# Performance work log

Hardware: AMD Instinct MI355X
Metric: run time of the kernel (lower is better)

The kernel has to match this reference:

```python
import jax, jax.numpy as jnp
import numpy as np

N, E = 20000, 320000
D, H, DFF, EDIM, L = 256, 8, 1024, 16, 4
C = D // H  # head dim = 32
INPUT_DIM, EMB_DIM = 64, 64
EPS = 1e-5


def ln(x, g, b):
    mu = jnp.mean(x, axis=-1, keepdims=True)
    var = jnp.mean((x - mu) ** 2, axis=-1, keepdims=True)
    return (x - mu) * jax.lax.rsqrt(var + EPS) * g + b


def segment_softmax(alpha, seg, num_segments):
    # alpha: [E, H], seg: [E] destination node ids
    m = jax.ops.segment_max(alpha, seg, num_segments=num_segments)
    m = jnp.where(jnp.isfinite(m), m, 0.0)
    ex = jnp.exp(alpha - m[seg])
    s = jax.ops.segment_sum(ex, seg, num_segments=num_segments)
    return ex / (s[seg] + 1e-16)


def transformer_conv(x, edge_attr, src, dst, Wq, bq, Wk, bk, Wv, bv, We, Wskip, bskip):
    # PyG TransformerConv: heads=H, concat=True, root_weight=True, beta=False
    q = (x @ Wq + bq).reshape(N, H, C)
    k = (x @ Wk + bk).reshape(N, H, C)
    v = (x @ Wv + bv).reshape(N, H, C)
    e = (edge_attr @ We).reshape(E, H, C)  # lin_edge has no bias
    kj = k[src] + e                         # [E,H,C]
    alpha = jnp.einsum('ehc,ehc->eh', q[dst], kj) / np.sqrt(C)
    alpha = segment_softmax(alpha, dst, N)  # softmax over incoming edges
    msg = (v[src] + e) * alpha[:, :, None]  # [E,H,C]
    out = jax.ops.segment_sum(msg, dst, num_segments=N).reshape(N, H * C)
    return out + x @ Wskip + bskip          # root/skip connection


def setup_inputs() -> dict:
    key = jax.random.key(0)
    ks = jax.random.split(key, 40)
    s = 0.02
    inp = {
        'input': jax.random.normal(ks[0], (N, INPUT_DIM), jnp.float32),
        'node_embedding': jax.random.normal(ks[1], (N, EMB_DIM), jnp.float32),
        'edge_attr': jax.random.normal(ks[2], (E, EDIM), jnp.float32),
        'edge_index': jax.random.randint(ks[3], (2, E), 0, N, jnp.int64)
          if jax.config.jax_enable_x64 else jax.random.randint(ks[3], (2, E), 0, N, jnp.int32),
        'Win': jax.random.normal(ks[4], (INPUT_DIM, D)) * s, 'b_in': jnp.zeros(D),
        'Wemb': jax.random.normal(ks[5], (EMB_DIM, D)) * s, 'bemb': jnp.zeros(D),
        'Wfus': jax.random.normal(ks[6], (3 * D, D)) * s, 'bfus': jnp.zeros(D),
        'Wq': jax.random.normal(ks[7], (L, D, D)) * s, 'bq': jnp.zeros((L, D)),
        'Wk': jax.random.normal(ks[8], (L, D, D)) * s, 'bk': jnp.zeros((L, D)),
        'Wv': jax.random.normal(ks[9], (L, D, D)) * s, 'bv': jnp.zeros((L, D)),
        'We': jax.random.normal(ks[10], (L, EDIM, D)) * s,
        'Wskip': jax.random.normal(ks[11], (L, D, D)) * s, 'bskip': jnp.zeros((L, D)),
        'n1g': jnp.ones((L, D)), 'n1b': jnp.zeros((L, D)),
        'W1f': jax.random.normal(ks[12], (L, D, DFF)) * s, 'b1f': jnp.zeros((L, DFF)),
        'W2f': jax.random.normal(ks[13], (L, DFF, D)) * s, 'b2f': jnp.zeros((L, D)),
        'n2g': jnp.ones((L, D)), 'n2b': jnp.zeros((L, D)),
        'fng': jnp.ones(D), 'fnb': jnp.zeros(D),
    }
    return inp


def reference(input, node_embedding, edge_attr, edge_index, Win, b_in, Wemb, bemb,
              Wfus, bfus, Wq, bq, Wk, bk, Wv, bv, We, Wskip, bskip, n1g, n1b,
              W1f, b1f, W2f, b2f, n2g, n2b, fng, fnb):
    src, dst = edge_index[0], edge_index[1]
    inp_proj = input @ Win + b_in           # [N,D]
    emb_proj = node_embedding @ Wemb + bemb  # [N,D]
    x = emb_proj
    for l in range(L):
        combined = jnp.concatenate([x, inp_proj, emb_proj], axis=-1)  # [N,3D]
        x = combined @ Wfus + bfus
        # layer: prenorm attn + residual, prenorm FFN + residual (dropout=0)
        xn = ln(x, n1g[l], n1b[l])
        x2 = transformer_conv(xn, edge_attr, src, dst, Wq[l], bq[l], Wk[l], bk[l],
                              Wv[l], bv[l], We[l], Wskip[l], bskip[l])
        x = x + x2
        xn = ln(x, n2g[l], n2b[l])
        x2 = jax.nn.relu(xn @ W1f[l] + b1f[l]) @ W2f[l] + b2f[l]
        x = x + x2
    return ln(x, fng, fnb)
```

## Files before the change

### kernel.cpp

```cpp
#include <hip/hip_runtime.h>
#include <math.h>

#define NN   20000
#define EE   320000
#define DD   256
#define HH   8
#define CC   32
#define DFFN 1024
#define LLAY 4
#define INDIM 64

typedef _Float16 f16;
typedef __attribute__((ext_vector_type(8))) _Float16 f16x8;
typedef __attribute__((ext_vector_type(4))) _Float16 f16x4;
typedef __attribute__((ext_vector_type(4))) float    f32x4;

template<int MODE, bool FUSED>
__global__ __launch_bounds__(256)
void hgemm_k(const f16* __restrict__ A0, const f16* __restrict__ A1,
             const f16* __restrict__ A2, const f16* __restrict__ Wt,
             const float* __restrict__ bias, float* __restrict__ outF,
             f16* __restrict__ outH, f16* __restrict__ outH2,
             int M, int K, int Nout)
{
    __shared__ f16 Af[4 * 64 * 8];
    __shared__ f16 Bf[4 * 128 * 8];

    const int tid  = threadIdx.x;
    const int wid  = tid >> 6;
    const int lane = tid & 63;
    const int g    = lane >> 4;
    const int ln   = lane & 15;
    const int WR   = wid >> 1;
    const int WC   = wid & 1;
    const int bm   = blockIdx.x * 64;
    const int bn   = blockIdx.y * 128;

    f32x4 acc[2][4];
#pragma unroll
    for (int m = 0; m < 2; ++m)
#pragma unroll
        for (int n = 0; n < 4; ++n) acc[m][n] = (f32x4){0.f, 0.f, 0.f, 0.f};

    const int ar = tid >> 2;
    const int ac = tid & 3;

    for (int k0 = 0; k0 < K; k0 += 32) {
        f16x8 av = {};
        {
            const int grow = bm + ar;
            if (grow < M) {
                const f16* gsrc;
                if (FUSED) {
                    const int kg  = k0 + ac * 8;
                    const int sel = kg >> 8;
                    const f16* Asrc = (sel == 0) ? A0 : ((sel == 1) ? A1 : A2);
                    gsrc = Asrc + (size_t)grow * 256 + (kg & 255);
                } else {
                    gsrc = A0 + (size_t)grow * K + k0 + ac * 8;
                }
                av = *(const f16x8*)gsrc;
            }
        }
        f16x8 bv0, bv1;
        {
            const int s0 = tid;
            const int s1 = tid + 256;
            bv0 = *(const f16x8*)(Wt + ((size_t)((k0 >> 3) + (s0 >> 7)) * Nout + bn + (s0 & 127)) * 8);
            bv1 = *(const f16x8*)(Wt + ((size_t)((k0 >> 3) + (s1 >> 7)) * Nout + bn + (s1 & 127)) * 8);
        }

        __syncthreads();
        *(f16x8*)&Af[(ac * 64 + ar) * 8] = av;
        *(f16x8*)&Bf[(size_t)tid * 8]         = bv0;
        *(f16x8*)&Bf[(size_t)(tid + 256) * 8] = bv1;
        __syncthreads();

        f16x8 af[2], bf[4];
#pragma unroll
        for (int m = 0; m < 2; ++m)
            af[m] = *(const f16x8*)&Af[(g * 64 + WR * 32 + m * 16 + ln) * 8];
#pragma unroll
        for (int n = 0; n < 4; ++n)
            bf[n] = *(const f16x8*)&Bf[(g * 128 + WC * 64 + n * 16 + ln) * 8];
#pragma unroll
        for (int m = 0; m < 2; ++m)
#pragma unroll
            for (int n = 0; n < 4; ++n)
                acc[m][n] = __builtin_amdgcn_mfma_f32_16x16x32_f16(af[m], bf[n], acc[m][n], 0, 0, 0);
    }

    float bvv[4];
#pragma unroll
    for (int n = 0; n < 4; ++n) bvv[n] = bias[bn + WC * 64 + n * 16 + ln];

#pragma unroll
    for (int m = 0; m < 2; ++m) {
        const int rbase = bm + WR * 32 + m * 16 + g * 4;
#pragma unroll
        for (int reg = 0; reg < 4; ++reg) {
            const int row = rbase + reg;
            if (row >= M) continue;
#pragma unroll
            for (int n = 0; n < 4; ++n) {
                const int col = bn + WC * 64 + n * 16 + ln;
                float v = acc[m][n][reg] + bvv[n];
                const size_t idx = (size_t)row * Nout + col;
                if (MODE == 0) {
                    outF[idx] = v;
                } else if (MODE == 1) {
                    outH[idx] = (f16)fmaxf(v, 0.f);
                } else if (MODE == 2) {
                    const float nv = outF[idx] + v;
                    outF[idx] = nv;
                    outH2[idx] = (f16)nv;
                } else {
                    outH[idx] = (f16)v;
                }
            }
        }
    }
}

__global__ __launch_bounds__(256)
void cvtW_k(const float* __restrict__ W, f16* __restrict__ Wt, int K, int N)
{
    const size_t lo  = (size_t)blockIdx.y * K * N;
    const int    idx = blockIdx.x * 256 + threadIdx.x;
    const int    k   = idx / N;
    const int    n   = idx - k * N;
    Wt[lo + ((size_t)(k >> 3) * N + n) * 8 + (k & 7)] = (f16)W[lo + idx];
}

__global__ __launch_bounds__(256)
void cvtW4_k(const float* __restrict__ Wq, const float* __restrict__ Wk,
             const float* __restrict__ Wv, const float* __restrict__ Ws,
             const float* __restrict__ bq, const float* __restrict__ bk,
             const float* __restrict__ bv, const float* __restrict__ bs,
             f16* __restrict__ Wt, float* __restrict__ bout)
{
    const int l   = blockIdx.y;
    const int idx = blockIdx.x * 256 + threadIdx.x;
    const int k   = idx >> 10;
    const int n   = idx & 1023;
    const int m   = n >> 8;
    const int c   = n & 255;
    const float* src = (m == 0) ? Wq : (m == 1) ? Wk : (m == 2) ? Wv : Ws;
    const float  v   = src[(size_t)l * 65536 + k * 256 + c];
    Wt[(size_t)l * 262144 + ((size_t)(k >> 3) * 1024 + n) * 8 + (k & 7)] = (f16)v;
    if (k == 0) {
        const float* bsrc = (m == 0) ? bq : (m == 1) ? bk : (m == 2) ? bv : bs;
        bout[l * 1024 + n] = bsrc[l * 256 + c];
    }
}

__global__ __launch_bounds__(256)
void cvt_act_k(const float* __restrict__ in, f16* __restrict__ out, int n)
{
    const int i = (blockIdx.x * 256 + threadIdx.x) * 4;
    if (i < n) {
        const float4 v = *(const float4*)&in[i];
        f16x4 o = {(f16)v.x, (f16)v.y, (f16)v.z, (f16)v.w};
        *(f16x4*)&out[i] = o;
    }
}

template<typename T>
__global__ __launch_bounds__(256)
void ln_k(const float* __restrict__ in, const float* __restrict__ g,
          const float* __restrict__ b, T* __restrict__ out, int M)
{
    const int wave = threadIdx.x >> 6;
    const int lane = threadIdx.x & 63;
    const int row  = blockIdx.x * 4 + wave;
    if (row >= M) return;

    const float4 v = *(const float4*)&in[(size_t)row * DD + lane * 4];
    float s = v.x + v.y + v.z + v.w;
#pragma unroll
    for (int off = 32; off; off >>= 1) s += __shfl_xor(s, off, 64);
    const float mu = s * (1.f / 256.f);

    const float dx = v.x - mu, dy = v.y - mu, dz = v.z - mu, dw = v.w - mu;
    float q = dx*dx + dy*dy + dz*dz + dw*dw;
#pragma unroll
    for (int off = 32; off; off >>= 1) q += __shfl_xor(q, off, 64);
    const float rs = rsqrtf(q * (1.f / 256.f) + 1e-5f);

    const float4 gv = *(const float4*)&g[lane * 4];
    const float4 bv = *(const float4*)&b[lane * 4];
    const float ox = dx * rs * gv.x + bv.x;
    const float oy = dy * rs * gv.y + bv.y;
    const float oz = dz * rs * gv.z + bv.z;
    const float ow = dw * rs * gv.w + bv.w;
    if constexpr (sizeof(T) == 2) {
        f16x4 o = {(f16)ox, (f16)oy, (f16)oz, (f16)ow};
        *(f16x4*)&out[(size_t)row * DD + lane * 4] = o;
    } else {
        float4 o = {ox, oy, oz, ow};
        *(float4*)&out[(size_t)row * DD + lane * 4] = o;
    }
}

__global__ void hist_k(const int* __restrict__ dst, int* __restrict__ cnt)
{
    const int e = blockIdx.x * blockDim.x + threadIdx.x;
    if (e < EE) atomicAdd(&cnt[dst[e]], 1);
}

__global__ __launch_bounds__(256)
void scan_k(const int* __restrict__ cnt, int* __restrict__ row_ptr,
            int* __restrict__ cursor)
{
    __shared__ int sums[256];
    const int t  = threadIdx.x;
    const int CH = (NN + 255) / 256;
    const int s0 = t * CH;
    const int s1 = min(s0 + CH, NN);

    int s = 0;
    for (int i = s0; i < s1; ++i) s += cnt[i];
    sums[t] = s;
    __syncthreads();
    for (int off = 1; off < 256; off <<= 1) {
        const int v = (t >= off) ? sums[t - off] : 0;
        __syncthreads();
        sums[t] += v;
        __syncthreads();
    }
    int run = (t == 0) ? 0 : sums[t - 1];
    for (int i = s0; i < s1; ++i) {
        row_ptr[i] = run;
        cursor[i]  = run;
        run += cnt[i];
    }
    if (t == 255) row_ptr[NN] = run;
}

__global__ void scatter_k(const int* __restrict__ dst, int* __restrict__ cursor,
                          int* __restrict__ eids)
{
    const int e = blockIdx.x * blockDim.x + threadIdx.x;
    if (e < EE) {
        const int idx = atomicAdd(&cursor[dst[e]], 1);
        eids[idx] = e;
    }
}

__global__ __launch_bounds__(256)
void edge_attn_k(const f16* __restrict__ qkvs, const float* __restrict__ edge_attr,
                 const float* __restrict__ Wel, const int* __restrict__ row_ptr,
                 const int* __restrict__ eids, const int* __restrict__ srcarr,
                 float* __restrict__ x)
{
    const int i   = blockIdx.x;
    const int tid = threadIdx.x;

    float wc[16];
#pragma unroll
    for (int t = 0; t < 16; ++t) wc[t] = Wel[t * DD + tid];

    const float qv = (float)qkvs[(size_t)i * 1024 + tid] * 0.17677669529663687f;

    float m = -INFINITY, s = 0.f, acc = 0.f;
    const int jbeg = row_ptr[i];
    const int jend = row_ptr[i + 1];

    int j = jbeg;
    for (; j + 1 < jend; j += 2) {
        const int e0 = eids[j],     e1 = eids[j + 1];
        const int s0 = srcarr[e0],  s1 = srcarr[e1];

        const float4* ea0p = (const float4*)(edge_attr + (size_t)e0 * 16);
        const float4* ea1p = (const float4*)(edge_attr + (size_t)e1 * 16);
        const float4 a00 = ea0p[0], a01 = ea0p[1], a02 = ea0p[2], a03 = ea0p[3];
        const float4 a10 = ea1p[0], a11 = ea1p[1], a12 = ea1p[2], a13 = ea1p[3];
        float kv0 = (float)qkvs[(size_t)s0 * 1024 + 256 + tid];
        float vv0 = (float)qkvs[(size_t)s0 * 1024 + 512 + tid];
        float kv1 = (float)qkvs[(size_t)s1 * 1024 + 256 + tid];
        float vv1 = (float)qkvs[(size_t)s1 * 1024 + 512 + tid];

        const float ev0 =
            a00.x*wc[0]  + a00.y*wc[1]  + a00.z*wc[2]  + a00.w*wc[3]  +
            a01.x*wc[4]  + a01.y*wc[5]  + a01.z*wc[6]  + a01.w*wc[7]  +
            a02.x*wc[8]  + a02.y*wc[9]  + a02.z*wc[10] + a02.w*wc[11] +
            a03.x*wc[12] + a03.y*wc[13] + a03.z*wc[14] + a03.w*wc[15];
        const float ev1 =
            a10.x*wc[0]  + a10.y*wc[1]  + a10.z*wc[2]  + a10.w*wc[3]  +
            a11.x*wc[4]  + a11.y*wc[5]  + a11.z*wc[6]  + a11.w*wc[7]  +
            a12.x*wc[8]  + a12.y*wc[9]  + a12.z*wc[10] + a12.w*wc[11] +
            a13.x*wc[12] + a13.y*wc[13] + a13.z*wc[14] + a13.w*wc[15];
        kv0 += ev0; vv0 += ev0;
        kv1 += ev1; vv1 += ev1;

        float d0 = qv * kv0;
        float d1 = qv * kv1;
#pragma unroll
        for (int off = 16; off; off >>= 1) {
            d0 += __shfl_xor(d0, off, 32);
            d1 += __shfl_xor(d1, off, 32);
        }

        const float mn   = fmaxf(m, fmaxf(d0, d1));
        const float corr = __expf(m - mn);
        const float p0   = __expf(d0 - mn);
        const float p1   = __expf(d1 - mn);
        s   = s * corr + p0 + p1;
        acc = acc * corr + p0 * vv0 + p1 * vv1;
        m   = mn;
    }
    if (j < jend) {
        const int e  = eids[j];
        const int sj = srcarr[e];
        const float4* eap = (const float4*)(edge_attr + (size_t)e * 16);
        const float4 ea0 = eap[0], ea1 = eap[1], ea2 = eap[2], ea3 = eap[3];
        float kv = (float)qkvs[(size_t)sj * 1024 + 256 + tid];
        float vv = (float)qkvs[(size_t)sj * 1024 + 512 + tid];
        const float ev =
            ea0.x*wc[0]  + ea0.y*wc[1]  + ea0.z*wc[2]  + ea0.w*wc[3]  +
            ea1.x*wc[4]  + ea1.y*wc[5]  + ea1.z*wc[6]  + ea1.w*wc[7]  +
            ea2.x*wc[8]  + ea2.y*wc[9]  + ea2.z*wc[10] + ea2.w*wc[11] +
            ea3.x*wc[12] + ea3.y*wc[13] + ea3.z*wc[14] + ea3.w*wc[15];
        kv += ev; vv += ev;
        float a = qv * kv;
#pragma unroll
        for (int off = 16; off; off >>= 1) a += __shfl_xor(a, off, 32);
        const float mn   = fmaxf(m, a);
        const float corr = __expf(m - mn);
        const float p    = __expf(a - mn);
        s   = s * corr + p;
        acc = acc * corr + p * vv;
        m   = mn;
    }

    const float msg = acc / (s + 1e-16f);
    const size_t o  = (size_t)i * DD + tid;
    x[o] += msg + (float)qkvs[(size_t)i * 1024 + 768 + tid];
}

extern "C" void kernel_launch(void* const* d_in, const int* in_sizes, int n_in,
                              void* d_out, int out_size, void* d_ws, size_t ws_size,
                              hipStream_t stream)
{
    const float* input = (const float*)d_in[0];
    const float* nemb  = (const float*)d_in[1];
    const float* eattr = (const float*)d_in[2];
    const int*   eidx  = (const int*)d_in[3];
    const float* Win   = (const float*)d_in[4];
    const float* b_in  = (const float*)d_in[5];
    const float* Wemb  = (const float*)d_in[6];
    const float* bemb  = (const float*)d_in[7];
    const float* Wfus  = (const float*)d_in[8];
    const float* bfus  = (const float*)d_in[9];
    const float* Wq    = (const float*)d_in[10];
    const float* bq    = (const float*)d_in[11];
    const float* Wk    = (const float*)d_in[12];
    const float* bk    = (const float*)d_in[13];
    const float* Wv    = (const float*)d_in[14];
    const float* bv    = (const float*)d_in[15];
    const float* We    = (const float*)d_in[16];
    const float* Wskip = (const float*)d_in[17];
    const float* bskip = (const float*)d_in[18];
    const float* n1g   = (const float*)d_in[19];
    const float* n1b   = (const float*)d_in[20];
    const float* W1f   = (const float*)d_in[21];
    const float* b1f   = (const float*)d_in[22];
    const float* W2f   = (const float*)d_in[23];
    const float* b2f   = (const float*)d_in[24];
    const float* n2g   = (const float*)d_in[25];
    const float* n2b   = (const float*)d_in[26];
    const float* fng   = (const float*)d_in[27];
    const float* fnb   = (const float*)d_in[28];

    const int* srcarr = eidx;
    const int* dstarr = eidx + EE;

    char* p = (char*)d_ws;
    auto alloc = [&](size_t bytes) { char* r = p; p += (bytes + 255) & ~(size_t)255; return r; };
    const size_t ND = (size_t)NN * DD;
    float* xA      = (float*)alloc(ND * 4);
    f16*   h_inp   = (f16*)alloc(ND * 2);
    f16*   h_emb   = (f16*)alloc(ND * 2);
    f16*   h_x     = (f16*)alloc(ND * 2);
    f16*   xn_h    = (f16*)alloc(ND * 2);
    f16*   qkvs_h  = (f16*)alloc((size_t)NN * 1024 * 2);
    f16*   mid_h   = qkvs_h;
    f16*   h_input = (f16*)alloc((size_t)NN * INDIM * 2);
    f16*   h_nemb  = (f16*)alloc((size_t)NN * INDIM * 2);
    f16*   Wt_in   = (f16*)alloc((size_t)INDIM * DD * 2);
    f16*   Wt_emb  = (f16*)alloc((size_t)INDIM * DD * 2);
    f16*   Wt_fus  = (f16*)alloc((size_t)768 * DD * 2);
    f16*   Wt_pack = (f16*)alloc((size_t)LLAY * DD * 1024 * 2);
    f16*   Wt_f1   = (f16*)alloc((size_t)LLAY * DD * DFFN * 2);
    f16*   Wt_f2   = (f16*)alloc((size_t)LLAY * DFFN * DD * 2);
    float* bpack   = (float*)alloc((size_t)LLAY * 1024 * 4);
    int*   cnt     = (int*)alloc(NN * 4);
    int*   cursor  = (int*)alloc(NN * 4);
    int*   row_ptr = (int*)alloc((NN + 1) * 4);
    int*   eids    = (int*)alloc(EE * 4);

    const int  lnGrid = (NN + 3) / 4;
    const dim3 gS(313, 2);
    const dim3 gW(313, 8);

    hipMemsetAsync(cnt, 0, NN * sizeof(int), stream);
    cvtW_k<<<dim3(INDIM * DD / 256, 1), 256, 0, stream>>>(Win,  Wt_in,  INDIM, DD);
    cvtW_k<<<dim3(INDIM * DD / 256, 1), 256, 0, stream>>>(Wemb, Wt_emb, INDIM, DD);
    cvtW_k<<<dim3(768 * DD / 256,  1), 256, 0, stream>>>(Wfus, Wt_fus, 768, DD);
    cvtW_k<<<dim3(DD * DFFN / 256, LLAY), 256, 0, stream>>>(W1f,  Wt_f1,  DD, DFFN);
    cvtW_k<<<dim3(DFFN * DD / 256, LLAY), 256, 0, stream>>>(W2f,  Wt_f2,  DFFN, DD);
    cvtW4_k<<<dim3(DD * 1024 / 256, LLAY), 256, 0, stream>>>(Wq, Wk, Wv, Wskip,
                                                             bq, bk, bv, bskip, Wt_pack, bpack);
    cvt_act_k<<<NN * INDIM / 4 / 256, 256, 0, stream>>>(input, h_input, NN * INDIM);
    cvt_act_k<<<NN * INDIM / 4 / 256, 256, 0, stream>>>(nemb,  h_nemb,  NN * INDIM);

    hgemm_k<3,false><<<gS, 256, 0, stream>>>(h_input, nullptr, nullptr, Wt_in,  b_in,
                                             nullptr, h_inp, nullptr, NN, INDIM, DD);
    hgemm_k<3,false><<<gS, 256, 0, stream>>>(h_nemb,  nullptr, nullptr, Wt_emb, bemb,
                                             nullptr, h_emb, nullptr, NN, INDIM, DD);
    hist_k<<<EE / 256, 256, 0, stream>>>(dstarr, cnt);
    scan_k<<<1, 256, 0, stream>>>(cnt, row_ptr, cursor);
    scatter_k<<<EE / 256, 256, 0, stream>>>(dstarr, cursor, eids);

    for (int l = 0; l < LLAY; ++l) {
        const f16* hx_l = (l == 0) ? h_emb : h_x;

        hgemm_k<0,true><<<gS, 256, 0, stream>>>(hx_l, h_inp, h_emb,
            Wt_fus, bfus, xA, nullptr, nullptr, NN, 768, DD);
        ln_k<f16><<<lnGrid, 256, 0, stream>>>(xA, n1g + l * DD, n1b + l * DD, xn_h, NN);
        hgemm_k<3,false><<<gW, 256, 0, stream>>>(xn_h, nullptr, nullptr,
            Wt_pack + (size_t)l * DD * 1024, bpack + l * 1024, nullptr, qkvs_h, nullptr, NN, DD, 1024);
        edge_attn_k<<<NN, 256, 0, stream>>>(qkvs_h, eattr, We + (size_t)l * 16 * DD,
                                            row_ptr, eids, srcarr, xA);
        ln_k<f16><<<lnGrid, 256, 0, stream>>>(xA, n2g + l * DD, n2b + l * DD, xn_h, NN);
        hgemm_k<1,false><<<gW, 256, 0, stream>>>(xn_h, nullptr, nullptr,
            Wt_f1 + (size_t)l * DD * DFFN, b1f + l * DFFN, nullptr, mid_h, nullptr, NN, DD, DFFN);
        hgemm_k<2,false><<<gS, 256, 0, stream>>>(mid_h, nullptr, nullptr,
            Wt_f2 + (size_t)l * DFFN * DD, b2f + l * DD, xA, nullptr, h_x, NN, DFFN, DD);
    }

    ln_k<float><<<lnGrid, 256, 0, stream>>>(xA, fng, fnb, (float*)d_out, NN);
}
```

Before: 1.264 ms.

## Load GEMM tiles directly into LDS and use 128-row tiles for wide GEMMs

Replaces the register-staged global-to-LDS copies in the fp16 MFMA GEMM with global_load_lds direct transfers. This removes the VGPR round trip and one barrier per k-step, at the cost of a trailing barrier. Adds a BM template parameter so the QKV-skip and FFN1 GEMMs (N=1024) use 128-row tiles, which doubles MFMA work per B-tile load and halves the grid. Out-of-range rows are now clamped to M-1 instead of zero-filled. The direct LDS load relies on each wave writing a contiguous 64x16B chunk, which matches the layout used.

After: 1.291 ms. 2.2% more time.

```diff
diff --git a/kernel.cpp b/kernel.cpp
--- a/kernel.cpp
+++ b/kernel.cpp
@@ -15,7 +15,7 @@
 typedef __attribute__((ext_vector_type(4))) _Float16 f16x4;
 typedef __attribute__((ext_vector_type(4))) float    f32x4;
 
-template<int MODE, bool FUSED>
+template<int MODE, int BM, bool FUSED>
 __global__ __launch_bounds__(256)
 void hgemm_k(const f16* __restrict__ A0, const f16* __restrict__ A1,
              const f16* __restrict__ A2, const f16* __restrict__ Wt,
@@ -23,7 +23,8 @@
              f16* __restrict__ outH, f16* __restrict__ outH2,
              int M, int K, int Nout)
 {
-    __shared__ f16 Af[4 * 64 * 8];
+    constexpr int MF = BM / 32;
+    __shared__ f16 Af[4 * BM * 8];
     __shared__ f16 Bf[4 * 128 * 8];
 
     const int tid  = threadIdx.x;
@@ -33,61 +34,80 @@
     const int ln   = lane & 15;
     const int WR   = wid >> 1;
     const int WC   = wid & 1;
-    const int bm   = blockIdx.x * 64;
+    const int bm   = blockIdx.x * BM;
     const int bn   = blockIdx.y * 128;
 
-    f32x4 acc[2][4];
-#pragma unroll
-    for (int m = 0; m < 2; ++m)
+    f32x4 acc[MF][4];
+#pragma unroll
+    for (int m = 0; m < MF; ++m)
 #pragma unroll
         for (int n = 0; n < 4; ++n) acc[m][n] = (f32x4){0.f, 0.f, 0.f, 0.f};
 
-    const int ar = tid >> 2;
-    const int ac = tid & 3;
-
     for (int k0 = 0; k0 < K; k0 += 32) {
-        f16x8 av = {};
-        {
-            const int grow = bm + ar;
-            if (grow < M) {
+        if (BM == 128) {
+#pragma unroll
+            for (int t = 0; t < 2; ++t) {
+                const int ia = wid + t * 4;
+                const int c = ia & 3, rb = ia >> 2;
+                int grow = bm + rb * 64 + lane;
+                grow = grow < M ? grow : (M - 1);
                 const f16* gsrc;
                 if (FUSED) {
-                    const int kg  = k0 + ac * 8;
+                    const int kg  = k0 + c * 8;
                     const int sel = kg >> 8;
                     const f16* Asrc = (sel == 0) ? A0 : ((sel == 1) ? A1 : A2);
                     gsrc = Asrc + (size_t)grow * 256 + (kg & 255);
                 } else {
-                    gsrc = A0 + (size_t)grow * K + k0 + ac * 8;
+                    gsrc = A0 + (size_t)grow * K + k0 + c * 8;
                 }
-                av = *(const f16x8*)gsrc;
+                __builtin_amdgcn_global_load_lds(
+                    (const __attribute__((address_space(1))) void*)gsrc,
+                    (__attribute__((address_space(3))) void*)&Af[(c * 128 + rb * 64) * 8],
+                    16, 0, 0);
             }
+        } else {
+            const int c = wid;
+            int grow = bm + lane;
+            grow = grow < M ? grow : (M - 1);
+            const f16* gsrc;
+            if (FUSED) {
+                const int kg  = k0 + c * 8;
+                const int sel = kg >> 8;
+                const f16* Asrc = (sel == 0) ? A0 : ((sel == 1) ? A1 : A2);
+                gsrc = Asrc + (size_t)grow * 256 + (kg & 255);
+            } else {
+                gsrc = A0 + (size_t)grow * K + k0 + c * 8;
+            }
+            __builtin_amdgcn_global_load_lds(
+                (const __attribute__((address_space(1))) void*)gsrc,
+                (__attribute__((address_space(3))) void*)&Af[(c * 64) * 8],
+                16, 0, 0);
         }
-        f16x8 bv0, bv1;
-        {
-            const int s0 = tid;
-            const int s1 = tid + 256;
-            bv0 = *(const f16x8*)(Wt + ((size_t)((k0 >> 3) + (s0 >> 7)) * Nout + bn + (s0 & 127)) * 8);
-            bv1 = *(const f16x8*)(Wt + ((size_t)((k0 >> 3) + (s1 >> 7)) * Nout + bn + (s1 & 127)) * 8);
+#pragma unroll
+        for (int t = 0; t < 2; ++t) {
+            const int ib = wid + t * 4;
+            const int c = ib & 3, cb = ib >> 2;
+            const f16* gsrc = Wt + ((size_t)((k0 >> 3) + c) * Nout + bn + cb * 64 + lane) * 8;
+            __builtin_amdgcn_global_load_lds(
+                (const __attribute__((address_space(1))) void*)gsrc,
+                (__attribute__((address_space(3))) void*)&Bf[(c * 128 + cb * 64) * 8],
+                16, 0, 0);
         }
-
         __syncthreads();
-        *(f16x8*)&Af[(ac * 64 + ar) * 8] = av;
-        *(f16x8*)&Bf[(size_t)tid * 8]         = bv0;
-        *(f16x8*)&Bf[(size_t)(tid + 256) * 8] = bv1;
-        __syncthreads();
-
-        f16x8 af[2], bf[4];
-#pragma unroll
-        for (int m = 0; m < 2; ++m)
-            af[m] = *(const f16x8*)&Af[(g * 64 + WR * 32 + m * 16 + ln) * 8];
+
+        f16x8 af[MF], bf[4];
+#pragma unroll
+        for (int m = 0; m < MF; ++m)
+            af[m] = *(const f16x8*)&Af[(g * BM + WR * (BM / 2) + m * 16 + ln) * 8];
 #pragma unroll
         for (int n = 0; n < 4; ++n)
             bf[n] = *(const f16x8*)&Bf[(g * 128 + WC * 64 + n * 16 + ln) * 8];
 #pragma unroll
-        for (int m = 0; m < 2; ++m)
+        for (int m = 0; m < MF; ++m)
 #pragma unroll
             for (int n = 0; n < 4; ++n)
                 acc[m][n] = __builtin_amdgcn_mfma_f32_16x16x32_f16(af[m], bf[n], acc[m][n], 0, 0, 0);
+        __syncthreads();
     }
 
     float bvv[4];
@@ -95,8 +115,8 @@
     for (int n = 0; n < 4; ++n) bvv[n] = bias[bn + WC * 64 + n * 16 + ln];
 
 #pragma unroll
-    for (int m = 0; m < 2; ++m) {
-        const int rbase = bm + WR * 32 + m * 16 + g * 4;
+    for (int m = 0; m < MF; ++m) {
+        const int rbase = bm + WR * (BM / 2) + m * 16 + g * 4;
 #pragma unroll
         for (int reg = 0; reg < 4; ++reg) {
             const int row = rbase + reg;
@@ -401,7 +421,7 @@
 
     const int  lnGrid = (NN + 3) / 4;
     const dim3 gS(313, 2);
-    const dim3 gW(313, 8);
+    const dim3 gW(157, 8);
 
     hipMemsetAsync(cnt, 0, NN * sizeof(int), stream);
     cvtW_k<<<dim3(INDIM * DD / 256, 1), 256, 0, stream>>>(Win,  Wt_in,  INDIM, DD);
@@ -414,10 +434,10 @@
     cvt_act_k<<<NN * INDIM / 4 / 256, 256, 0, stream>>>(input, h_input, NN * INDIM);
     cvt_act_k<<<NN * INDIM / 4 / 256, 256, 0, stream>>>(nemb,  h_nemb,  NN * INDIM);
 
-    hgemm_k<3,false><<<gS, 256, 0, stream>>>(h_input, nullptr, nullptr, Wt_in,  b_in,
-                                             nullptr, h_inp, nullptr, NN, INDIM, DD);
-    hgemm_k<3,false><<<gS, 256, 0, stream>>>(h_nemb,  nullptr, nullptr, Wt_emb, bemb,
-                                             nullptr, h_emb, nullptr, NN, INDIM, DD);
+    hgemm_k<3,64,false><<<gS, 256, 0, stream>>>(h_input, nullptr, nullptr, Wt_in,  b_in,
+                                                nullptr, h_inp, nullptr, NN, INDIM, DD);
+    hgemm_k<3,64,false><<<gS, 256, 0, stream>>>(h_nemb,  nullptr, nullptr, Wt_emb, bemb,
+                                                nullptr, h_emb, nullptr, NN, INDIM, DD);
     hist_k<<<EE / 256, 256, 0, stream>>>(dstarr, cnt);
     scan_k<<<1, 256, 0, stream>>>(cnt, row_ptr, cursor);
     scatter_k<<<EE / 256, 256, 0, stream>>>(dstarr, cursor, eids);
@@ -425,17 +445,17 @@
     for (int l = 0; l < LLAY; ++l) {
         const f16* hx_l = (l == 0) ? h_emb : h_x;
 
-        hgemm_k<0,true><<<gS, 256, 0, stream>>>(hx_l, h_inp, h_emb,
+        hgemm_k<0,64,true><<<gS, 256, 0, stream>>>(hx_l, h_inp, h_emb,
             Wt_fus, bfus, xA, nullptr, nullptr, NN, 768, DD);
         ln_k<f16><<<lnGrid, 256, 0, stream>>>(xA, n1g + l * DD, n1b + l * DD, xn_h, NN);
-        hgemm_k<3,false><<<gW, 256, 0, stream>>>(xn_h, nullptr, nullptr,
+        hgemm_k<3,128,false><<<gW, 256, 0, stream>>>(xn_h, nullptr, nullptr,
             Wt_pack + (size_t)l * DD * 1024, bpack + l * 1024, nullptr, qkvs_h, nullptr, NN, DD, 1024);
         edge_attn_k<<<NN, 256, 0, stream>>>(qkvs_h, eattr, We + (size_t)l * 16 * DD,
                                             row_ptr, eids, srcarr, xA);
         ln_k<f16><<<lnGrid, 256, 0, stream>>>(xA, n2g + l * DD, n2b + l * DD, xn_h, NN);
-        hgemm_k<1,false><<<gW, 256, 0, stream>>>(xn_h, nullptr, nullptr,
+        hgemm_k<1,128,false><<<gW, 256, 0, stream>>>(xn_h, nullptr, nullptr,
             Wt_f1 + (size_t)l * DD * DFFN, b1f + l * DFFN, nullptr, mid_h, nullptr, NN, DD, DFFN);
-        hgemm_k<2,false><<<gS, 256, 0, stream>>>(mid_h, nullptr, nullptr,
+        hgemm_k<2,64,false><<<gS, 256, 0, stream>>>(mid_h, nullptr, nullptr,
             Wt_f2 + (size_t)l * DFFN * DD, b2f + l * DD, xA, nullptr, h_x, NN, DFFN, DD);
     }
 
```

## Factor edge projection out of per-edge attention loop via q·We and weighted attr sums

Applied to the files above, without the earlier changes.

Instead of projecting each edge's 16-dim attribute to 256 dims inside the edge loop, the kernel precomputes q·We per head (16 values) so the edge term of the score is a 16-term dot product handled by lane-level shuffles. It also accumulates a softmax-weighted sum of raw edge attributes per head and applies We once at the end. This removes about 16 FMAs per thread per edge and the float4 loads of the full attribute row, at the cost of two block barriers, some shared memory and an extra running accumulator.

Result: no change. 1.277 ms (+1.0%).

```diff
diff --git a/kernel.cpp b/kernel.cpp
--- a/kernel.cpp
+++ b/kernel.cpp
@@ -253,16 +253,35 @@
                  const int* __restrict__ eids, const int* __restrict__ srcarr,
                  float* __restrict__ x)
 {
+    __shared__ float qwe[128];
+    __shared__ float wea_s[128];
+
     const int i   = blockIdx.x;
     const int tid = threadIdx.x;
-
-    float wc[16];
-#pragma unroll
-    for (int t = 0; t < 16; ++t) wc[t] = Wel[t * DD + tid];
-
+    const int h   = tid >> 5;
+    const int c   = tid & 31;
+
+    if (tid < 128) {
+        const int hh = tid >> 4, tt = tid & 15;
+        const f16*   qrow = qkvs + (size_t)i * 1024 + hh * 32;
+        const float* wrow = Wel + tt * 256 + hh * 32;
+        const f16x8* q8 = (const f16x8*)qrow;
+        float a0 = 0.f;
+#pragma unroll
+        for (int b = 0; b < 4; ++b) {
+            const f16x8 qq = q8[b];
+#pragma unroll
+            for (int u = 0; u < 8; ++u)
+                a0 = fmaf((float)qq[u], wrow[b * 8 + u], a0);
+        }
+        qwe[tid] = a0 * 0.17677669529663687f;
+    }
     const float qv = (float)qkvs[(size_t)i * 1024 + tid] * 0.17677669529663687f;
-
-    float m = -INFINITY, s = 0.f, acc = 0.f;
+    __syncthreads();
+
+    const float qwv = (c < 16) ? qwe[h * 16 + c] : 0.f;
+
+    float m = -INFINITY, s = 0.f, acc = 0.f, wea = 0.f;
     const int jbeg = row_ptr[i];
     const int jend = row_ptr[i + 1];
 
@@ -271,30 +290,15 @@
         const int e0 = eids[j],     e1 = eids[j + 1];
         const int s0 = srcarr[e0],  s1 = srcarr[e1];
 
-        const float4* ea0p = (const float4*)(edge_attr + (size_t)e0 * 16);
-        const float4* ea1p = (const float4*)(edge_attr + (size_t)e1 * 16);
-        const float4 a00 = ea0p[0], a01 = ea0p[1], a02 = ea0p[2], a03 = ea0p[3];
-        const float4 a10 = ea1p[0], a11 = ea1p[1], a12 = ea1p[2], a13 = ea1p[3];
-        float kv0 = (float)qkvs[(size_t)s0 * 1024 + 256 + tid];
-        float vv0 = (float)qkvs[(size_t)s0 * 1024 + 512 + tid];
-        float kv1 = (float)qkvs[(size_t)s1 * 1024 + 256 + tid];
-        float vv1 = (float)qkvs[(size_t)s1 * 1024 + 512 + tid];
-
-        const float ev0 =
-            a00.x*wc[0]  + a00.y*wc[1]  + a00.z*wc[2]  + a00.w*wc[3]  +
-            a01.x*wc[4]  + a01.y*wc[5]  + a01.z*wc[6]  + a01.w*wc[7]  +
-            a02.x*wc[8]  + a02.y*wc[9]  + a02.z*wc[10] + a02.w*wc[11] +
-            a03.x*wc[12] + a03.y*wc[13] + a03.z*wc[14] + a03.w*wc[15];
-        const float ev1 =
-            a10.x*wc[0]  + a10.y*wc[1]  + a10.z*wc[2]  + a10.w*wc[3]  +
-            a11.x*wc[4]  + a11.y*wc[5]  + a11.z*wc[6]  + a11.w*wc[7]  +
-            a12.x*wc[8]  + a12.y*wc[9]  + a12.z*wc[10] + a12.w*wc[11] +
-            a13.x*wc[12] + a13.y*wc[13] + a13.z*wc[14] + a13.w*wc[15];
-        kv0 += ev0; vv0 += ev0;
-        kv1 += ev1; vv1 += ev1;
-
-        float d0 = qv * kv0;
-        float d1 = qv * kv1;
+        const float ea0 = edge_attr[(size_t)e0 * 16 + (c & 15)];
+        const float ea1 = edge_attr[(size_t)e1 * 16 + (c & 15)];
+        const float kv0 = (float)qkvs[(size_t)s0 * 1024 + 256 + tid];
+        const float vv0 = (float)qkvs[(size_t)s0 * 1024 + 512 + tid];
+        const float kv1 = (float)qkvs[(size_t)s1 * 1024 + 256 + tid];
+        const float vv1 = (float)qkvs[(size_t)s1 * 1024 + 512 + tid];
+
+        float d0 = fmaf(qv, kv0, qwv * ea0);
+        float d1 = fmaf(qv, kv1, qwv * ea1);
 #pragma unroll
         for (int off = 16; off; off >>= 1) {
             d0 += __shfl_xor(d0, off, 32);
@@ -305,35 +309,37 @@
         const float corr = __expf(m - mn);
         const float p0   = __expf(d0 - mn);
         const float p1   = __expf(d1 - mn);
-        s   = s * corr + p0 + p1;
+        s   = s   * corr + p0 + p1;
         acc = acc * corr + p0 * vv0 + p1 * vv1;
+        wea = wea * corr + p0 * ea0 + p1 * ea1;
         m   = mn;
     }
     if (j < jend) {
         const int e  = eids[j];
         const int sj = srcarr[e];
-        const float4* eap = (const float4*)(edge_attr + (size_t)e * 16);
-        const float4 ea0 = eap[0], ea1 = eap[1], ea2 = eap[2], ea3 = eap[3];
-        float kv = (float)qkvs[(size_t)sj * 1024 + 256 + tid];
-        float vv = (float)qkvs[(size_t)sj * 1024 + 512 + tid];
-        const float ev =
-            ea0.x*wc[0]  + ea0.y*wc[1]  + ea0.z*wc[2]  + ea0.w*wc[3]  +
-            ea1.x*wc[4]  + ea1.y*wc[5]  + ea1.z*wc[6]  + ea1.w*wc[7]  +
-            ea2.x*wc[8]  + ea2.y*wc[9]  + ea2.z*wc[10] + ea2.w*wc[11] +
-            ea3.x*wc[12] + ea3.y*wc[13] + ea3.z*wc[14] + ea3.w*wc[15];
-        kv += ev; vv += ev;
-        float a = qv * kv;
-#pragma unroll
-        for (int off = 16; off; off >>= 1) a += __shfl_xor(a, off, 32);
-        const float mn   = fmaxf(m, a);
+        const float ea = edge_attr[(size_t)e * 16 + (c & 15)];
+        const float kv = (float)qkvs[(size_t)sj * 1024 + 256 + tid];
+        const float vv = (float)qkvs[(size_t)sj * 1024 + 512 + tid];
+        float d = fmaf(qv, kv, qwv * ea);
+#pragma unroll
+        for (int off = 16; off; off >>= 1) d += __shfl_xor(d, off, 32);
+        const float mn   = fmaxf(m, d);
         const float corr = __expf(m - mn);
-        const float p    = __expf(a - mn);
-        s   = s * corr + p;
+        const float p    = __expf(d - mn);
+        s   = s   * corr + p;
         acc = acc * corr + p * vv;
+        wea = wea * corr + p * ea;
         m   = mn;
     }
 
-    const float msg = acc / (s + 1e-16f);
+    if (c < 16) wea_s[h * 16 + c] = wea;
+    __syncthreads();
+    float ve = 0.f;
+#pragma unroll
+    for (int t = 0; t < 16; ++t)
+        ve = fmaf(wea_s[h * 16 + t], Wel[t * DD + tid], ve);
+
+    const float msg = (acc + ve) / (s + 1e-16f);
     const size_t o  = (size_t)i * DD + tid;
     x[o] += msg + (float)qkvs[(size_t)i * 1024 + 768 + tid];
 }
```
